# Kernel optimization log

Hardware: AMD Instinct MI355X
Metric: run time of the kernel (lower is better)

Reference implementation:

```python
import jax, jax.numpy as jnp
import numpy as np

GRID = 16          # control-point lattice (16x16 points -> 450 triangles)
H_IMG = W_IMG = 384


def _grid_mesh(h, w, g):
    ys, xs = np.meshgrid(np.linspace(0, h - 1, g), np.linspace(0, w - 1, g), indexing='ij')
    pts = np.stack([xs.ravel(), ys.ravel()], axis=1).astype(np.float32)  # [g*g, 2] (x, y)
    faces = []
    for i in range(g - 1):
        for j in range(g - 1):
            a = i * g + j
            b = a + 1
            c = a + g
            d = c + 1
            faces.append([a, b, c])
            faces.append([b, d, c])
    return pts, np.asarray(faces, dtype=np.int32)


def setup_inputs() -> dict:
    key = jax.random.key(0)
    k1, k2 = jax.random.split(key)
    base, faces = _grid_mesh(H_IMG, W_IMG, GRID)
    # warped screen-space points; UVs stay on the regular lattice -> texture warp
    jitter = np.asarray(jax.random.normal(k1, base.shape, jnp.float32)) * 4.0
    points = np.clip(base + jitter, 0.0, np.array([W_IMG - 1, H_IMG - 1], np.float32))
    image = jax.random.uniform(k2, (1, H_IMG, W_IMG, 3), jnp.float32)
    return {
        'points': jnp.asarray(points),
        'uv_points': jnp.asarray(base),
        'image': image,
        'faces': jnp.asarray(faces),
    }


def _render(points, uv_points, image, faces):
    img = image[0]                       # [H, W, C]
    H, W, C = img.shape
    eps = 1e-8
    tol = 1e-7
    wh = jnp.array([W - 1, H - 1], jnp.float32)

    # normalized_points (ratio == 1 for square image): pixel -> NDC
    pn = (points / wh * 2.0 - 1.0) * jnp.array([(W - 1) / W, (H - 1) / H], jnp.float32)
    fv = pn[faces]                       # [F, 3, 2]
    v0, v1, v2 = fv[:, 0], fv[:, 1], fv[:, 2]

    # pixel centers in the same NDC convention
    xs = 2.0 * (jnp.arange(W, dtype=jnp.float32) + 0.5) / W - 1.0
    ys = 2.0 * (jnp.arange(H, dtype=jnp.float32) + 0.5) / H - 1.0
    PX, PY = jnp.meshgrid(xs, ys)        # [H, W]
    px = PX.reshape(-1, 1)               # [HW, 1]
    py = PY.reshape(-1, 1)

    def edge_fn(a, b):                   # signed area of (a, b, p) per pixel/face -> [HW, F]
        return (b[:, 0] - a[:, 0]) * (py - a[:, 1]) - (b[:, 1] - a[:, 1]) * (px - a[:, 0])

    area = (v1[:, 0] - v0[:, 0]) * (v2[:, 1] - v0[:, 1]) - (v1[:, 1] - v0[:, 1]) * (v2[:, 0] - v0[:, 0])
    inv_area = 1.0 / jnp.where(jnp.abs(area) < eps, 1.0, area)

    w0 = edge_fn(v1, v2) * inv_area      # barycentric coords, [HW, F]
    w1 = edge_fn(v2, v0) * inv_area
    w2 = edge_fn(v0, v1) * inv_area

    inside = (w0 >= -tol) & (w1 >= -tol) & (w2 >= -tol) & (jnp.abs(area) >= eps)
    hit = inside.any(axis=1)             # [HW]
    fidx = jnp.argmax(inside, axis=1)    # first covering face (faces_per_pixel=1, constant z)

    take = lambda w: jnp.take_along_axis(w, fidx[:, None], axis=1)[:, 0]
    bary = jnp.stack([take(w0), take(w1), take(w2)], axis=-1)  # [HW, 3]

    # verts_uvs: uv_points / [W-1, H-1], gathered per face, interpolated per pixel
    face_uv = (uv_points / wh)[faces]    # [F, 3, 2]
    uv = jnp.einsum('pk,pkd->pd', bary, face_uv[fidx])         # [HW, 2] in [0, 1]

    # bilinear texture sample
    x = jnp.clip(uv[:, 0] * (W - 1), 0.0, W - 1)
    y = jnp.clip(uv[:, 1] * (H - 1), 0.0, H - 1)
    x0 = jnp.floor(x).astype(jnp.int32)
    y0 = jnp.floor(y).astype(jnp.int32)
    x1 = jnp.minimum(x0 + 1, W - 1)
    y1 = jnp.minimum(y0 + 1, H - 1)
    fx = (x - x0.astype(jnp.float32))[:, None]
    fy = (y - y0.astype(jnp.float32))[:, None]
    color = (img[y0, x0] * (1 - fx) * (1 - fy) + img[y0, x1] * fx * (1 - fy)
             + img[y1, x0] * (1 - fx) * fy + img[y1, x1] * fx * fy)     # [HW, C]

    return jnp.where(hit[:, None], color, 0.0).reshape(H, W, C)


def reference(points, uv_points, image, faces):
    return _render(points, uv_points, image, faces)
```

## Files before the change

kernel.cpp:

```cpp
#include <hip/hip_runtime.h>


#define NF_MAX 450
#define WIMG 384
#define HIMG 384
#define MARGIN 1e-4f

__device__ __forceinline__ float fbar(float r) {
    asm volatile("" : "+v"(r));
    return r;
}
__device__ __forceinline__ float mulb(float a, float b) { return fbar(a * b); }

__global__ __launch_bounds__(256)
void wm_fused(const float* __restrict__ points,
              const float* __restrict__ uvp,
              const int*   __restrict__ faces,
              int nf,
              const float* __restrict__ img,
              float* __restrict__ out)
{
    __shared__ float  flds[NF_MAX * 16];
    __shared__ float4 fbbox[NF_MAX];
    __shared__ unsigned long long masks[8];
    __shared__ int    list[NF_MAX];

    const int tid = threadIdx.x;

    const float sc = (float)(383.0 / 384.0);
    for (int f = tid; f < nf; f += 256) {
        int idx[3] = { faces[f*3+0], faces[f*3+1], faces[f*3+2] };

        float v[3][2], uv[3][2];
        #pragma unroll
        for (int k = 0; k < 3; ++k) {
            float px = points[idx[k]*2 + 0];
            float py = points[idx[k]*2 + 1];
            v[k][0] = fbar(fbar(fbar(px / 383.0f) * 2.0f - 1.0f) * sc);
            v[k][1] = fbar(fbar(fbar(py / 383.0f) * 2.0f - 1.0f) * sc);
            uv[k][0] = fbar(uvp[idx[k]*2 + 0] / 383.0f);
            uv[k][1] = fbar(uvp[idx[k]*2 + 1] / 383.0f);
        }

        float area = fbar(mulb(v[1][0]-v[0][0], v[2][1]-v[0][1])
                        - mulb(v[1][1]-v[0][1], v[2][0]-v[0][0]));
        bool  valid    = (fabsf(area) >= 1e-8f);
        float inv_area = fbar(1.0f / (valid ? area : 1.0f));

        float* o = &flds[f * 16];
        o[0]=v[0][0]; o[1]=v[0][1]; o[2]=v[1][0]; o[3]=v[1][1];
        o[4]=v[2][0]; o[5]=v[2][1]; o[6]=inv_area; o[7]=0.0f;
        o[8]=uv[0][0]; o[9]=uv[0][1]; o[10]=uv[1][0]; o[11]=uv[1][1];
        o[12]=uv[2][0]; o[13]=uv[2][1];

        float4 bb;
        if (valid) {
            bb.x = fminf(fminf(v[0][0], v[1][0]), v[2][0]);
            bb.y = fminf(fminf(v[0][1], v[1][1]), v[2][1]);
            bb.z = fmaxf(fmaxf(v[0][0], v[1][0]), v[2][0]);
            bb.w = fmaxf(fmaxf(v[0][1], v[1][1]), v[2][1]);
        } else {
            bb.x = 1e30f; bb.y = 1e30f; bb.z = -1e30f; bb.w = -1e30f;
        }
        fbbox[f] = bb;
    }
    __syncthreads();

    const int lx = tid & 15, ly = tid >> 4;
    const int c0 = blockIdx.x * 16, r0 = blockIdx.y * 16;
    const int col = c0 + lx, row = r0 + ly;

    const float tx_lo = 2.0f * ((float)c0 + 0.5f)  / 384.0f - 1.0f - MARGIN;
    const float tx_hi = 2.0f * ((float)c0 + 15.5f) / 384.0f - 1.0f + MARGIN;
    const float ty_lo = 2.0f * ((float)r0 + 0.5f)  / 384.0f - 1.0f - MARGIN;
    const float ty_hi = 2.0f * ((float)r0 + 15.5f) / 384.0f - 1.0f + MARGIN;

    bool pred[2];
    #pragma unroll
    for (int r = 0; r < 2; ++r) {
        int f = r * 256 + tid;
        bool p = false;
        if (f < nf) {
            float4 bb = fbbox[f];
            p = (bb.x <= tx_hi) & (bb.z >= tx_lo) & (bb.y <= ty_hi) & (bb.w >= ty_lo);
        }
        pred[r] = p;
        unsigned long long m = __ballot(p);
        if ((tid & 63) == 0) masks[r * 4 + (tid >> 6)] = m;
    }
    __syncthreads();

    int ncand = 0;
    #pragma unroll
    for (int k = 0; k < 8; ++k) ncand += __popcll(masks[k]);

    const int lane = tid & 63;
    const unsigned long long below = (lane == 0) ? 0ULL : ((1ULL << lane) - 1ULL);
    #pragma unroll
    for (int r = 0; r < 2; ++r) {
        if (pred[r]) {
            int w = r * 4 + (tid >> 6);
            int pos = __popcll(masks[w] & below);
            for (int k = 0; k < w; ++k) pos += __popcll(masks[k]);
            list[pos] = r * 256 + tid;
        }
    }
    __syncthreads();

    const float px = fbar(fbar(2.0f * ((float)col + 0.5f) / 384.0f) - 1.0f);
    const float py = fbar(fbar(2.0f * ((float)row + 0.5f) / 384.0f) - 1.0f);

    int   hitoff = -1;
    float b0 = 0.0f, b1 = 0.0f, b2 = 0.0f;

    for (int i = 0; i < ncand; ++i) {
        const float* fd = &flds[list[i] * 16];
        const float v0x = fd[0], v0y = fd[1];
        const float v1x = fd[2], v1y = fd[3];
        const float v2x = fd[4], v2y = fd[5];
        const float ia  = fd[6];

        float e0 = fbar(mulb(v2x - v1x, py - v1y) - mulb(v2y - v1y, px - v1x));
        float e1 = fbar(mulb(v0x - v2x, py - v2y) - mulb(v0y - v2y, px - v2x));
        float e2 = fbar(mulb(v1x - v0x, py - v0y) - mulb(v1y - v0y, px - v0x));

        float w0 = mulb(e0, ia);
        float w1 = mulb(e1, ia);
        float w2 = mulb(e2, ia);

        if (w0 >= -1e-7f && w1 >= -1e-7f && w2 >= -1e-7f) {
            hitoff = list[i] * 16; b0 = w0; b1 = w1; b2 = w2;
            break;
        }
    }

    float c0f = 0.0f, c1f = 0.0f, c2f = 0.0f;
    if (hitoff >= 0) {
        const float* fd = &flds[hitoff];
        float ux = b0 * fd[8] + b1 * fd[10] + b2 * fd[12];
        float uy = b0 * fd[9] + b1 * fd[11] + b2 * fd[13];

        float x = fminf(fmaxf(ux * 383.0f, 0.0f), 383.0f);
        float y = fminf(fmaxf(uy * 383.0f, 0.0f), 383.0f);
        int x0 = (int)floorf(x);
        int y0 = (int)floorf(y);
        int x1 = min(x0 + 1, 383);
        int y1 = min(y0 + 1, 383);
        float fx = x - (float)x0;
        float fy = y - (float)y0;

        const float* p00 = &img[(y0 * WIMG + x0) * 3];
        const float* p10 = &img[(y0 * WIMG + x1) * 3];
        const float* p01 = &img[(y1 * WIMG + x0) * 3];
        const float* p11 = &img[(y1 * WIMG + x1) * 3];

        float w00 = (1.0f - fx) * (1.0f - fy);
        float w10 = fx * (1.0f - fy);
        float w01 = (1.0f - fx) * fy;
        float w11 = fx * fy;

        c0f = p00[0]*w00 + p10[0]*w10 + p01[0]*w01 + p11[0]*w11;
        c1f = p00[1]*w00 + p10[1]*w10 + p01[1]*w01 + p11[1]*w11;
        c2f = p00[2]*w00 + p10[2]*w10 + p01[2]*w01 + p11[2]*w11;
    }

    const int p = row * WIMG + col;
    out[p * 3 + 0] = c0f;
    out[p * 3 + 1] = c1f;
    out[p * 3 + 2] = c2f;
}

extern "C" void kernel_launch(void* const* d_in, const int* in_sizes, int n_in,
                              void* d_out, int out_size, void* d_ws, size_t ws_size,
                              hipStream_t stream) {
    const float* points = (const float*)d_in[0];
    const float* uvp    = (const float*)d_in[1];
    const float* img    = (const float*)d_in[2];
    const int*   faces  = (const int*)d_in[3];

    int nf = in_sizes[3] / 3;
    if (nf > NF_MAX) nf = NF_MAX;

    hipLaunchKernelGGL(wm_fused, dim3(WIMG / 16, HIMG / 16), dim3(256), 0, stream,
                       points, uvp, faces, nf, img, (float*)d_out);
}
```

Before: 12.85 us.

## Stage vertices in LDS once and fuse face setup into bbox culling pass

Each thread now transforms one vertex (NDC and UV) into shared memory instead of every face gathering and transforming three vertices from global memory. Per-face setup (area, inverse area, uv copy) moves into the bbox culling loop, which drops the separate bbox array and one pass over faces. The face record stride changes from 16 to 17 floats to reduce LDS bank conflicts in the candidate loop. Vertex count is capped at 256, so larger meshes would break.

```diff
diff --git a/kernel.cpp b/kernel.cpp
--- a/kernel.cpp
+++ b/kernel.cpp
@@ -2,9 +2,11 @@
 
 
 #define NF_MAX 450
+#define NP_MAX 256
 #define WIMG 384
 #define HIMG 384
 #define MARGIN 1e-4f
+#define FSTRIDE 17
 
 __device__ __forceinline__ float fbar(float r) {
     asm volatile("" : "+v"(r));
@@ -16,53 +18,25 @@
 void wm_fused(const float* __restrict__ points,
               const float* __restrict__ uvp,
               const int*   __restrict__ faces,
-              int nf,
+              int nf, int np,
               const float* __restrict__ img,
               float* __restrict__ out)
 {
-    __shared__ float  flds[NF_MAX * 16];
-    __shared__ float4 fbbox[NF_MAX];
+    __shared__ float vx[NP_MAX], vy[NP_MAX], tux[NP_MAX], tuy[NP_MAX];
+    __shared__ float flds[NF_MAX * FSTRIDE];
     __shared__ unsigned long long masks[8];
-    __shared__ int    list[NF_MAX];
+    __shared__ int   list[NF_MAX];
 
     const int tid = threadIdx.x;
+    const float sc = (float)(383.0 / 384.0);
 
-    const float sc = (float)(383.0 / 384.0);
-    for (int f = tid; f < nf; f += 256) {
-        int idx[3] = { faces[f*3+0], faces[f*3+1], faces[f*3+2] };
-
-        float v[3][2], uv[3][2];
-        #pragma unroll
-        for (int k = 0; k < 3; ++k) {
-            float px = points[idx[k]*2 + 0];
-            float py = points[idx[k]*2 + 1];
-            v[k][0] = fbar(fbar(fbar(px / 383.0f) * 2.0f - 1.0f) * sc);
-            v[k][1] = fbar(fbar(fbar(py / 383.0f) * 2.0f - 1.0f) * sc);
-            uv[k][0] = fbar(uvp[idx[k]*2 + 0] / 383.0f);
-            uv[k][1] = fbar(uvp[idx[k]*2 + 1] / 383.0f);
-        }
-
-        float area = fbar(mulb(v[1][0]-v[0][0], v[2][1]-v[0][1])
-                        - mulb(v[1][1]-v[0][1], v[2][0]-v[0][0]));
-        bool  valid    = (fabsf(area) >= 1e-8f);
-        float inv_area = fbar(1.0f / (valid ? area : 1.0f));
-
-        float* o = &flds[f * 16];
-        o[0]=v[0][0]; o[1]=v[0][1]; o[2]=v[1][0]; o[3]=v[1][1];
-        o[4]=v[2][0]; o[5]=v[2][1]; o[6]=inv_area; o[7]=0.0f;
-        o[8]=uv[0][0]; o[9]=uv[0][1]; o[10]=uv[1][0]; o[11]=uv[1][1];
-        o[12]=uv[2][0]; o[13]=uv[2][1];
-
-        float4 bb;
-        if (valid) {
-            bb.x = fminf(fminf(v[0][0], v[1][0]), v[2][0]);
-            bb.y = fminf(fminf(v[0][1], v[1][1]), v[2][1]);
-            bb.z = fmaxf(fmaxf(v[0][0], v[1][0]), v[2][0]);
-            bb.w = fmaxf(fmaxf(v[0][1], v[1][1]), v[2][1]);
-        } else {
-            bb.x = 1e30f; bb.y = 1e30f; bb.z = -1e30f; bb.w = -1e30f;
-        }
-        fbbox[f] = bb;
+    if (tid < np) {
+        float px = points[tid*2 + 0];
+        float py = points[tid*2 + 1];
+        vx[tid]  = fbar(fbar(fbar(px / 383.0f) * 2.0f - 1.0f) * sc);
+        vy[tid]  = fbar(fbar(fbar(py / 383.0f) * 2.0f - 1.0f) * sc);
+        tux[tid] = fbar(uvp[tid*2 + 0] / 383.0f);
+        tuy[tid] = fbar(uvp[tid*2 + 1] / 383.0f);
     }
     __syncthreads();
 
@@ -78,11 +52,37 @@
     bool pred[2];
     #pragma unroll
     for (int r = 0; r < 2; ++r) {
-        int f = r * 256 + tid;
+        const int f = r * 256 + tid;
         bool p = false;
         if (f < nf) {
-            float4 bb = fbbox[f];
-            p = (bb.x <= tx_hi) & (bb.z >= tx_lo) & (bb.y <= ty_hi) & (bb.w >= ty_lo);
+            int i0 = faces[f*3 + 0];
+            int i1 = faces[f*3 + 1];
+            int i2 = faces[f*3 + 2];
+
+            float v0x = vx[i0], v0y = vy[i0];
+            float v1x = vx[i1], v1y = vy[i1];
+            float v2x = vx[i2], v2y = vy[i2];
+
+            float area = fbar(mulb(v1x - v0x, v2y - v0y)
+                            - mulb(v1y - v0y, v2x - v0x));
+            bool  valid    = (fabsf(area) >= 1e-8f);
+            float inv_area = fbar(1.0f / (valid ? area : 1.0f));
+
+            float* o = &flds[f * FSTRIDE];
+            o[0] = v0x; o[1] = v0y; o[2] = v1x; o[3] = v1y;
+            o[4] = v2x; o[5] = v2y; o[6] = inv_area;
+            o[7]  = tux[i0]; o[8]  = tuy[i0];
+            o[9]  = tux[i1]; o[10] = tuy[i1];
+            o[11] = tux[i2]; o[12] = tuy[i2];
+
+            if (valid) {
+                float bxmin = fminf(fminf(v0x, v1x), v2x);
+                float bymin = fminf(fminf(v0y, v1y), v2y);
+                float bxmax = fmaxf(fmaxf(v0x, v1x), v2x);
+                float bymax = fmaxf(fmaxf(v0y, v1y), v2y);
+                p = (bxmin <= tx_hi) & (bxmax >= tx_lo)
+                  & (bymin <= ty_hi) & (bymax >= ty_lo);
+            }
         }
         pred[r] = p;
         unsigned long long m = __ballot(p);
@@ -114,7 +114,7 @@
     float b0 = 0.0f, b1 = 0.0f, b2 = 0.0f;
 
     for (int i = 0; i < ncand; ++i) {
-        const float* fd = &flds[list[i] * 16];
+        const float* fd = &flds[list[i] * FSTRIDE];
         const float v0x = fd[0], v0y = fd[1];
         const float v1x = fd[2], v1y = fd[3];
         const float v2x = fd[4], v2y = fd[5];
@@ -129,7 +129,7 @@
         float w2 = mulb(e2, ia);
 
         if (w0 >= -1e-7f && w1 >= -1e-7f && w2 >= -1e-7f) {
-            hitoff = list[i] * 16; b0 = w0; b1 = w1; b2 = w2;
+            hitoff = list[i] * FSTRIDE; b0 = w0; b1 = w1; b2 = w2;
             break;
         }
     }
@@ -137,8 +137,8 @@
     float c0f = 0.0f, c1f = 0.0f, c2f = 0.0f;
     if (hitoff >= 0) {
         const float* fd = &flds[hitoff];
-        float ux = b0 * fd[8] + b1 * fd[10] + b2 * fd[12];
-        float uy = b0 * fd[9] + b1 * fd[11] + b2 * fd[13];
+        float ux = b0 * fd[7] + b1 * fd[9]  + b2 * fd[11];
+        float uy = b0 * fd[8] + b1 * fd[10] + b2 * fd[12];
 
         float x = fminf(fmaxf(ux * 383.0f, 0.0f), 383.0f);
         float y = fminf(fmaxf(uy * 383.0f, 0.0f), 383.0f);
@@ -180,7 +180,9 @@
 
     int nf = in_sizes[3] / 3;
     if (nf > NF_MAX) nf = NF_MAX;
+    int np = in_sizes[0] / 2;
+    if (np > NP_MAX) np = NP_MAX;
 
     hipLaunchKernelGGL(wm_fused, dim3(WIMG / 16, HIMG / 16), dim3(256), 0, stream,
-                       points, uvp, faces, nf, img, (float*)d_out);
+                       points, uvp, faces, nf, np, img, (float*)d_out);
 }
```

New measurement: 10.87 us. -15.4%, faster.
